# Optimization experiments

Measured on AMD Instinct MI355X. Metric: run time of the kernel, lower is better.

## Reference

```python
import jax, jax.numpy as jnp
import numpy as np

B, LQ, LK, D = 64, 1024, 1024, 64
TEMPERATURE = 8.0  # sqrt(D)


def setup_inputs() -> dict:
    key = jax.random.key(0)
    k1, k2, k3, k4, k5, k6 = jax.random.split(key, 6)
    query = jax.random.normal(k1, (B, LQ, D), dtype=jnp.float32)
    key_t = jax.random.normal(k2, (B, LK, D), dtype=jnp.float32)
    value = jax.random.normal(k3, (B, LK, D), dtype=jnp.float32)
    query_mask = jax.random.uniform(k4, (B, LQ)) > 0.1
    key_mask = jax.random.uniform(k5, (B, LK)) > 0.1
    mask = jax.random.uniform(k6, (B, LQ, LK)) > 0.1
    return {"query": query, "key": key_t, "value": value,
            "query_mask": query_mask, "key_mask": key_mask, "mask": mask}


def reference(query, key, value, query_mask, key_mask, mask):
    # unnormalized score: bmm + scale + key/general masking with -inf
    attn = jnp.einsum('bqd,bkd->bqk', query, key) / TEMPERATURE
    neg_inf = jnp.array(-jnp.inf, dtype=attn.dtype)
    if key_mask is not None:
        attn = jnp.where(key_mask[:, None, :], attn, neg_inf)
    if mask is not None:
        attn = jnp.where(mask, attn, neg_inf)
    # softmax over key dim, then zero out masked queries
    attn = jax.nn.softmax(attn, axis=2)
    if query_mask is not None:
        attn = jnp.where(query_mask[:, :, None], attn, 0.0)
    attn_value = jnp.einsum('bqk,bkd->bqd', attn, value)
    return attn_value, attn
```

## Files before the change

### kernel.cpp

```cpp
#include <hip/hip_runtime.h>
#include <hip/hip_bf16.h>


#define NB   64
#define SLQ  1024
#define SLK  1024
#define DH   64
#define TQ   16
#define TK   64
#define NKT  16
#define PSTR 40
#define OSTR 68

typedef __attribute__((ext_vector_type(4))) float          f32x4;
typedef __attribute__((ext_vector_type(8))) __bf16         bf16x8;
typedef __attribute__((ext_vector_type(8))) unsigned short u16x8;

static __device__ __forceinline__ unsigned short f2bf(float f) {
  return __builtin_bit_cast(unsigned short, (__bf16)f);
}
static __device__ __forceinline__ bf16x8 cvt8(f32x4 a, f32x4 b) {
  bf16x8 r;
#pragma unroll
  for (int i = 0; i < 4; ++i) { r[i] = (__bf16)a[i]; r[i + 4] = (__bf16)b[i]; }
  return r;
}

__global__ __launch_bounds__(256, 3) void sdpa_fused(
    const float* __restrict__ Q, const float* __restrict__ K,
    const float* __restrict__ V, const int* __restrict__ QM,
    const int* __restrict__ KM, const int* __restrict__ MSK,
    float* __restrict__ OUT_AV, float* __restrict__ OUT_P) {
  const int g    = blockIdx.x;
  const int slot = g >> 3;
  const int b    = ((slot >> 6) << 3) | (g & 7);
  const int q0   = (slot & 63) * TQ;

  const int tid  = threadIdx.x;
  const int wave = tid >> 6;
  const int lane = tid & 63;
  const int col  = lane & 15;
  const int quad = lane >> 4;

  __shared__ __align__(16) unsigned char RAW[23168];
  float*          Ow = (float*)RAW + wave * (16 * OSTR);
  unsigned short* Pw = (unsigned short*)(RAW + 17408) + wave * (16 * PSTR);
  float* partM = (float*)(RAW + 22528);
  float* partL = partM + 64;
  float* rowM  = partL + 64;
  float* rowS  = rowM + 16;

  const size_t mbase = ((size_t)b * SLQ + q0) * SLK;

  const float* qp = Q + ((size_t)b * SLQ + q0 + col) * DH + quad * 8;
  bf16x8 aq0, aq1;
  {
    f32x4 a = *(const f32x4*)qp        * 0.125f;
    f32x4 c = *(const f32x4*)(qp + 4)  * 0.125f;
    f32x4 d = *(const f32x4*)(qp + 32) * 0.125f;
    f32x4 e = *(const f32x4*)(qp + 36) * 0.125f;
    aq0 = cvt8(a, c);
    aq1 = cvt8(d, e);
  }

  const float* kp  = K + ((size_t)b * SLK + wave * 16 + col) * DH + quad * 8;
  const int*   kmp = KM + b * SLK + wave * 16 + col;
  const int*   mkp = MSK + mbase + (size_t)(quad * 4) * SLK + wave * 16 + col;

  float sreg[NKT][4];
#pragma unroll
  for (int kt = 0; kt < NKT; ++kt) {
    const float* kq = kp + (size_t)kt * (TK * DH);
    f32x4 k0 = *(const f32x4*)kq;
    f32x4 k1 = *(const f32x4*)(kq + 4);
    f32x4 k2 = *(const f32x4*)(kq + 32);
    f32x4 k3 = *(const f32x4*)(kq + 36);
    const int km = kmp[kt * TK];
    int mr[4];
#pragma unroll
    for (int r = 0; r < 4; ++r)
      mr[r] = __builtin_nontemporal_load(mkp + (size_t)r * SLK + kt * TK);
    bf16x8 bk0 = cvt8(k0, k1);
    bf16x8 bk1 = cvt8(k2, k3);
    f32x4 acc = {0.f, 0.f, 0.f, 0.f};
    acc = __builtin_amdgcn_mfma_f32_16x16x32_bf16(aq0, bk0, acc, 0, 0, 0);
    acc = __builtin_amdgcn_mfma_f32_16x16x32_bf16(aq1, bk1, acc, 0, 0, 0);
#pragma unroll
    for (int r = 0; r < 4; ++r)
      sreg[kt][r] = (km && mr[r]) ? acc[r] : -INFINITY;
  }

  float Mw[4], Cr[4];
#pragma unroll
  for (int r = 0; r < 4; ++r) {
    float m = sreg[0][r];
#pragma unroll
    for (int kt = 1; kt < NKT; ++kt) m = fmaxf(m, sreg[kt][r]);
#pragma unroll
    for (int off = 1; off < 16; off <<= 1) m = fmaxf(m, __shfl_xor(m, off, 64));
    Mw[r] = m;
    const float mc = fmaxf(m, -1e30f);
    float l = 0.f;
#pragma unroll
    for (int kt = 0; kt < NKT; ++kt) {
      float e = __expf(sreg[kt][r] - mc);
      sreg[kt][r] = e;
      l += e;
    }
#pragma unroll
    for (int off = 1; off < 16; off <<= 1) l += __shfl_xor(l, off, 64);
    if (col == 0) {
      partM[wave * 16 + quad * 4 + r] = Mw[r];
      partL[wave * 16 + quad * 4 + r] = l;
    }
  }
  __syncthreads();
  if (tid < TQ) {
    float M = -INFINITY, L = 0.f;
#pragma unroll
    for (int w = 0; w < 4; ++w) {
      float m_ = partM[w * 16 + tid], l_ = partL[w * 16 + tid];
      float mn = fmaxf(M, m_);
      if (mn != -INFINITY) {
        L = L * __expf(M - mn) + l_ * __expf(m_ - mn);
        M = mn;
      }
    }
    rowM[tid] = fmaxf(M, -1e30f);
    rowS[tid] = (QM[b * SLQ + q0 + tid] && L > 0.f) ? (1.f / L) : 0.f;
  }
  __syncthreads();
#pragma unroll
  for (int r = 0; r < 4; ++r)
    Cr[r] = __expf(fmaxf(Mw[r], -1e30f) - rowM[quad * 4 + r]) * rowS[quad * 4 + r];

  const float* vp = V + ((size_t)b * SLK + wave * 16 + (quad & 1) * 8 +
                         (quad >> 1) * TK) * DH + col;
  float* outp = OUT_P + mbase + (size_t)(quad * 4) * SLK + wave * 16 + col;

  f32x4 acco[4] = {{0.f,0.f,0.f,0.f},{0.f,0.f,0.f,0.f},
                   {0.f,0.f,0.f,0.f},{0.f,0.f,0.f,0.f}};
#pragma unroll
  for (int st = 0; st < 8; ++st) {
    const int kt0 = st * 2, kt1 = kt0 + 1;
    float p0[4], p1[4];
#pragma unroll
    for (int r = 0; r < 4; ++r) {
      p0[r] = sreg[kt0][r] * Cr[r];
      p1[r] = sreg[kt1][r] * Cr[r];
      Pw[(quad * 4 + r) * PSTR + col]      = f2bf(p0[r]);
      Pw[(quad * 4 + r) * PSTR + 16 + col] = f2bf(p1[r]);
    }
#pragma unroll
    for (int r = 0; r < 4; ++r) {
      __builtin_nontemporal_store(p0[r], outp + (size_t)r * SLK + kt0 * TK);
      __builtin_nontemporal_store(p1[r], outp + (size_t)r * SLK + kt1 * TK);
    }

    const float* vq = vp + (size_t)st * (2 * TK * DH);
    float vv[4][8];
#pragma unroll
    for (int n0 = 0; n0 < 4; ++n0)
#pragma unroll
      for (int j = 0; j < 8; ++j)
        vv[n0][j] = vq[(size_t)j * DH + n0 * 16];

    bf16x8 ap = __builtin_bit_cast(bf16x8, *(const u16x8*)&Pw[col * PSTR + quad * 8]);
#pragma unroll
    for (int n0 = 0; n0 < 4; ++n0) {
      bf16x8 bv;
#pragma unroll
      for (int j = 0; j < 8; ++j) bv[j] = (__bf16)vv[n0][j];
      acco[n0] = __builtin_amdgcn_mfma_f32_16x16x32_bf16(ap, bv, acco[n0], 0, 0, 0);
    }
  }

#pragma unroll
  for (int n0 = 0; n0 < 4; ++n0)
#pragma unroll
    for (int r = 0; r < 4; ++r)
      Ow[(quad * 4 + r) * OSTR + n0 * 16 + col] = acco[n0][r];
  __syncthreads();
  {
    const int qq = tid >> 4, dd = (tid & 15) * 4;
    f32x4 s = {0.f, 0.f, 0.f, 0.f};
#pragma unroll
    for (int w = 0; w < 4; ++w) {
      const float* Os = (const float*)RAW + w * (16 * OSTR);
      s += *(const f32x4*)&Os[qq * OSTR + dd];
    }
    __builtin_nontemporal_store(s, (f32x4*)&OUT_AV[((size_t)b * SLQ + q0 + qq) * DH + dd]);
  }
}

extern "C" void kernel_launch(void* const* d_in, const int* in_sizes, int n_in,
                              void* d_out, int out_size, void* d_ws, size_t ws_size,
                              hipStream_t stream) {
  const float* q  = (const float*)d_in[0];
  const float* k  = (const float*)d_in[1];
  const float* v  = (const float*)d_in[2];
  const int*   qm = (const int*)d_in[3];
  const int*   km = (const int*)d_in[4];
  const int*   mk = (const int*)d_in[5];
  float* out_av = (float*)d_out;
  float* out_p  = out_av + (size_t)NB * SLQ * DH;
  sdpa_fused<<<dim3(NB * (SLQ / TQ)), dim3(256), 0, stream>>>(q, k, v, qm, km, mk, out_av, out_p);
}
```

Baseline: 667.8 us.

## Stage V through LDS with coalesced vector loads and register prefetch

```diff
diff --git a/kernel.cpp b/kernel.cpp
--- a/kernel.cpp
+++ b/kernel.cpp
@@ -9,12 +9,14 @@
 #define TQ   16
 #define TK   64
 #define NKT  16
+#define VSTR 76
 #define PSTR 40
 #define OSTR 68
 
 typedef __attribute__((ext_vector_type(4))) float          f32x4;
 typedef __attribute__((ext_vector_type(8))) __bf16         bf16x8;
 typedef __attribute__((ext_vector_type(8))) unsigned short u16x8;
+typedef __attribute__((ext_vector_type(4))) unsigned short u16x4;
 
 static __device__ __forceinline__ unsigned short f2bf(float f) {
   return __builtin_bit_cast(unsigned short, (__bf16)f);
@@ -24,6 +26,12 @@
 #pragma unroll
   for (int i = 0; i < 4; ++i) { r[i] = (__bf16)a[i]; r[i + 4] = (__bf16)b[i]; }
   return r;
+}
+static __device__ __forceinline__ u16x4 cvt4(f32x4 v) {
+  u16x4 h;
+#pragma unroll
+  for (int i = 0; i < 4; ++i) h[i] = f2bf(v[i]);
+  return h;
 }
 
 __global__ __launch_bounds__(256, 3) void sdpa_fused(
@@ -41,16 +49,20 @@
   const int lane = tid & 63;
   const int col  = lane & 15;
   const int quad = lane >> 4;
-
-  __shared__ __align__(16) unsigned char RAW[23168];
-  float*          Ow = (float*)RAW + wave * (16 * OSTR);
-  unsigned short* Pw = (unsigned short*)(RAW + 17408) + wave * (16 * PSTR);
-  float* partM = (float*)(RAW + 22528);
+  const int lrow = quad;
+  const int lc4  = col * 4;
+
+  __shared__ __align__(16) unsigned char RAW[25216];
+  unsigned short* Vw = (unsigned short*)(RAW + wave * (32 * VSTR * 2));
+  float*          Ow = (float*)(RAW + wave * (32 * VSTR * 2));
+  unsigned short* Pw = (unsigned short*)(RAW + 19456) + wave * (16 * PSTR);
+  float* partM = (float*)(RAW + 24576);
   float* partL = partM + 64;
   float* rowM  = partL + 64;
   float* rowS  = rowM + 16;
 
   const size_t mbase = ((size_t)b * SLQ + q0) * SLK;
+  const f32x4* vb4 = (const f32x4*)(V + (size_t)b * SLK * DH);
 
   const float* qp = Q + ((size_t)b * SLQ + q0 + col) * DH + quad * 8;
   bf16x8 aq0, aq1;
@@ -78,8 +90,7 @@
     const int km = kmp[kt * TK];
     int mr[4];
 #pragma unroll
-    for (int r = 0; r < 4; ++r)
-      mr[r] = __builtin_nontemporal_load(mkp + (size_t)r * SLK + kt * TK);
+    for (int r = 0; r < 4; ++r) mr[r] = mkp[(size_t)r * SLK + kt * TK];
     bf16x8 bk0 = cvt8(k0, k1);
     bf16x8 bk1 = cvt8(k2, k3);
     f32x4 acc = {0.f, 0.f, 0.f, 0.f};
@@ -89,6 +100,11 @@
     for (int r = 0; r < 4; ++r)
       sreg[kt][r] = (km && mr[r]) ? acc[r] : -INFINITY;
   }
+
+  f32x4 vreg[8];
+#pragma unroll
+  for (int j = 0; j < 8; ++j)
+    vreg[j] = vb4[(size_t)((j >> 2) * TK + wave * 16 + (j & 3) * 4 + lrow) * 16 + col];
 
   float Mw[4], Cr[4];
 #pragma unroll
@@ -134,8 +150,6 @@
   for (int r = 0; r < 4; ++r)
     Cr[r] = __expf(fmaxf(Mw[r], -1e30f) - rowM[quad * 4 + r]) * rowS[quad * 4 + r];
 
-  const float* vp = V + ((size_t)b * SLK + wave * 16 + (quad & 1) * 8 +
-                         (quad >> 1) * TK) * DH + col;
   float* outp = OUT_P + mbase + (size_t)(quad * 4) * SLK + wave * 16 + col;
 
   f32x4 acco[4] = {{0.f,0.f,0.f,0.f},{0.f,0.f,0.f,0.f},
@@ -143,6 +157,10 @@
 #pragma unroll
   for (int st = 0; st < 8; ++st) {
     const int kt0 = st * 2, kt1 = kt0 + 1;
+#pragma unroll
+    for (int j = 0; j < 8; ++j)
+      *(u16x4*)&Vw[(j * 4 + lrow) * VSTR + lc4] = cvt4(vreg[j]);
+
     float p0[4], p1[4];
 #pragma unroll
     for (int r = 0; r < 4; ++r) {
@@ -153,25 +171,26 @@
     }
 #pragma unroll
     for (int r = 0; r < 4; ++r) {
-      __builtin_nontemporal_store(p0[r], outp + (size_t)r * SLK + kt0 * TK);
-      __builtin_nontemporal_store(p1[r], outp + (size_t)r * SLK + kt1 * TK);
-    }
-
-    const float* vq = vp + (size_t)st * (2 * TK * DH);
-    float vv[4][8];
-#pragma unroll
-    for (int n0 = 0; n0 < 4; ++n0)
+      outp[(size_t)r * SLK + kt0 * TK] = p0[r];
+      outp[(size_t)r * SLK + kt1 * TK] = p1[r];
+    }
+
+    if (st < 7) {
 #pragma unroll
       for (int j = 0; j < 8; ++j)
-        vv[n0][j] = vq[(size_t)j * DH + n0 * 16];
+        vreg[j] = vb4[(size_t)((st * 2 + 2 + (j >> 2)) * TK + wave * 16 + (j & 3) * 4 + lrow) * 16
+                      + col];
+    }
 
     bf16x8 ap = __builtin_bit_cast(bf16x8, *(const u16x8*)&Pw[col * PSTR + quad * 8]);
 #pragma unroll
     for (int n0 = 0; n0 < 4; ++n0) {
-      bf16x8 bv;
-#pragma unroll
-      for (int j = 0; j < 8; ++j) bv[j] = (__bf16)vv[n0][j];
-      acco[n0] = __builtin_amdgcn_mfma_f32_16x16x32_bf16(ap, bv, acco[n0], 0, 0, 0);
+      u16x8 rv;
+#pragma unroll
+      for (int j = 0; j < 8; ++j)
+        rv[j] = Vw[(quad * 8 + j) * VSTR + n0 * 16 + col];
+      acco[n0] = __builtin_amdgcn_mfma_f32_16x16x32_bf16(
+          ap, __builtin_bit_cast(bf16x8, rv), acco[n0], 0, 0, 0);
     }
   }
 
@@ -186,10 +205,10 @@
     f32x4 s = {0.f, 0.f, 0.f, 0.f};
 #pragma unroll
     for (int w = 0; w < 4; ++w) {
-      const float* Os = (const float*)RAW + w * (16 * OSTR);
-      s += *(const f32x4*)&Os[qq * OSTR + dd];
-    }
-    __builtin_nontemporal_store(s, (f32x4*)&OUT_AV[((size_t)b * SLQ + q0 + qq) * DH + dd]);
+      const float* Os = (const float*)(RAW + w * (32 * VSTR * 2));
+      s += *(const f32x4*)&Os[(qq & 15) * OSTR + dd + (qq >> 4) * 0];
+    }
+    *(f32x4*)&OUT_AV[((size_t)b * SLQ + q0 + (qq & 15)) * DH + dd] = s;
   }
 }
 
```

New measurement: 625.4 us. -6.3%, faster.
